# Kernel optimization log

Measured on AMD Instinct MI355X. Metric: run time of the kernel, lower is better.

Reference implementation:

```python
import jax, jax.numpy as jnp
import numpy as np

B, T, D, E, C = 2, 2048, 2048, 8, 512
O1 = D // E  # per-expert hidden width (out_features // num_experts)


def setup_inputs() -> dict:
    key = jax.random.key(0)
    k = jax.random.split(key, 8)
    s = 1.0 / np.sqrt(D)
    return {
        "x": jax.random.normal(k[0], (B, T, D), dtype=jnp.float32),
        "dispatch_mask": jax.random.uniform(k[1], (B, T, E, C), dtype=jnp.float32),
        "combine_array": jax.random.uniform(k[2], (B, T, E, C), dtype=jnp.float32),
        # contract weights: nn.Linear(D, D) reshaped to (E, D//E, D)
        "W1": jax.random.uniform(k[3], (E, O1, D), jnp.float32, -s, s),
        "b1": jax.random.uniform(k[4], (E, O1), jnp.float32, -s, s),
        # expand weights: nn.Linear(D, D) reshaped to (E, D, D//E)
        "W2": jax.random.uniform(k[5], (E, D, O1), jnp.float32, -s, s),
        "b2": jax.random.uniform(k[6], (D,), jnp.float32, -s, s),
    }


def reference(x, dispatch_mask, combine_array, W1, b1, W2, b2):
    # --- ExpertsChooseMaskedContract ---
    # einsum('btd,btec,eod->beco') split into two GEMM-shaped contractions
    xe = jnp.einsum('btd,btec->becd', x, dispatch_mask)          # [B,E,C,D]
    h = jnp.einsum('becd,eod->beco', xe, W1) + b1[None, :, None, :]  # [B,E,C,O1]
    # --- GELU (torch nn.GELU default = exact erf form) ---
    h = jax.nn.gelu(h, approximate=False)
    # --- ExpertsChooseMaskedExpand (homogeneous-coords bias == add b2 then combine) ---
    y = jnp.einsum('beci,eoi->beco', h, W2) + b2[None, None, None, :]  # [B,E,C,D]
    out = jnp.einsum('beco,btec->bto', y, combine_array)          # [B,T,D]
    return out
```

## Files before the change

### kernel.cpp

```cpp
#include <hip/hip_runtime.h>
#include <math.h>

#define BB 2
#define TT 2048
#define DD 2048
#define EE 8
#define CCv 512
#define OO1 256

typedef unsigned short u16;
typedef __bf16 bf16x8 __attribute__((ext_vector_type(8)));
typedef float f32x4 __attribute__((ext_vector_type(4)));

__device__ __forceinline__ u16 f2bf(float f) {
    unsigned u = __float_as_uint(f);
    unsigned r = (u + 0x7fffu + ((u >> 16) & 1u)) >> 16;
    return (u16)r;
}

__device__ __forceinline__ void gload16(const void* g, void* s) {
    __builtin_amdgcn_global_load_lds(
        (const __attribute__((address_space(1))) void*)g,
        (__attribute__((address_space(3))) void*)s, 16, 0, 0);
}

__global__ __launch_bounds__(256) void conv_cast(const float* __restrict__ in,
                                                 u16* __restrict__ out, long n) {
    long i = ((long)blockIdx.x * 256 + threadIdx.x) * 4;
    float4 v = *(const float4*)&in[i];
    ushort4 o; o.x = f2bf(v.x); o.y = f2bf(v.y); o.z = f2bf(v.z); o.w = f2bf(v.w);
    *(ushort4*)&out[i] = o;
}

__global__ __launch_bounds__(256) void transpose_conv(
    const float* __restrict__ in, long inHi, long inLo, int modZ, long sIn,
    u16* __restrict__ out, long outZ, long sOut)
{
    __shared__ float tile[32][33];
    const int z = blockIdx.z;
    const float* ib = in + (long)(z / modZ) * inHi + (long)(z % modZ) * inLo;
    u16* ob = out + (long)z * outZ;
    const int t0 = blockIdx.y * 32, c0 = blockIdx.x * 32;
    const int tid = threadIdx.x;
    const int r = tid >> 3, c4 = (tid & 7) * 4;

    float4 v = *(const float4*)&ib[(long)(t0 + r) * sIn + c0 + c4];
    tile[r][c4 + 0] = v.x; tile[r][c4 + 1] = v.y;
    tile[r][c4 + 2] = v.z; tile[r][c4 + 3] = v.w;
    __syncthreads();

    const int oc = tid >> 3, t4 = (tid & 7) * 4;
    ushort4 o;
    o.x = f2bf(tile[t4 + 0][oc]);
    o.y = f2bf(tile[t4 + 1][oc]);
    o.z = f2bf(tile[t4 + 2][oc]);
    o.w = f2bf(tile[t4 + 3][oc]);
    *(ushort4*)&ob[(long)(c0 + oc) * sOut + t0 + t4] = o;
}

template<int EPI>
__global__ __launch_bounds__(256)
void mfma_gemm(const u16* __restrict__ A, long ldA, long aHi, long aLo, int modA,
               const u16* __restrict__ B, long ldB, long bHi, long bLo, int modB,
               void* __restrict__ Cout, long ldC, long cHi, long cLo, int modC,
               const float* __restrict__ bias, long biasLo, int modBias,
               int M, int N, int K)
{
    __shared__ __align__(16) char smem[32768];
    char* smA = smem;
    char* smB = smem + 16384;

    const int z = blockIdx.z;
    const char* Ab = (const char*)(A + (long)(z / modA) * aHi + (long)(z % modA) * aLo);
    const char* Bb = (const char*)(B + (long)(z / modB) * bHi + (long)(z % modB) * bLo);
    const long ldAb = ldA * 2, ldBb = ldB * 2;

    const int m0 = blockIdx.y * 128, n0 = blockIdx.x * 128;
    const int tid = threadIdx.x;
    const int l = tid & 63;
    const int w = tid >> 6;
    const int wm = w >> 1, wn = w & 1;

    const int srow = l >> 3;
    const int schunk = (l & 7) ^ srow;
    const int frow = l & 15;
    const int fgrp = l >> 4;
    const int fch0 = fgrp ^ (l & 7);

    int aoff[4], boff[4];
#pragma unroll
    for (int i = 0; i < 4; ++i) {
        aoff[i] = (wm * 64 + i * 16 + frow) * 128 + fch0 * 16;
        boff[i] = (wn * 64 + i * 16 + frow) * 128 + fch0 * 16;
    }

    f32x4 acc[4][4];
    const f32x4 zero4 = {0.f, 0.f, 0.f, 0.f};
#pragma unroll
    for (int i = 0; i < 4; ++i)
#pragma unroll
        for (int j = 0; j < 4; ++j) acc[i][j] = zero4;

    const long sgo = (long)schunk * 16;

    for (int k0 = 0; k0 < K; k0 += 64) {
        const long kb = (long)k0 * 2;
#pragma unroll
        for (int j = 0; j < 4; ++j) {
            const int rr = (j * 4 + w) * 8 + srow;
            gload16(Ab + (long)(m0 + rr) * ldAb + kb + sgo, smA + (j * 4 + w) * 1024);
            gload16(Bb + (long)(n0 + rr) * ldBb + kb + sgo, smB + (j * 4 + w) * 1024);
        }
        __syncthreads();
#pragma unroll
        for (int kk = 0; kk < 2; ++kk) {
            const int kx = kk * 64;
            bf16x8 af[4], bfr[4];
#pragma unroll
            for (int i = 0; i < 4; ++i) af[i] = *(const bf16x8*)(smA + (aoff[i] ^ kx));
#pragma unroll
            for (int i = 0; i < 4; ++i) bfr[i] = *(const bf16x8*)(smB + (boff[i] ^ kx));
#pragma unroll
            for (int mi = 0; mi < 4; ++mi)
#pragma unroll
                for (int ni = 0; ni < 4; ++ni)
                    acc[mi][ni] = __builtin_amdgcn_mfma_f32_16x16x32_bf16(
                        af[mi], bfr[ni], acc[mi][ni], 0, 0, 0);
        }
        __syncthreads();
    }

    const long cbase = (long)(z / modC) * cHi + (long)(z % modC) * cLo;
    const float* biasB = bias + (long)(z % modBias) * biasLo;
#pragma unroll
    for (int mi = 0; mi < 4; ++mi) {
#pragma unroll
        for (int ni = 0; ni < 4; ++ni) {
            const int col = n0 + wn * 64 + ni * 16 + frow;
            const int rowb = m0 + wm * 64 + mi * 16 + fgrp * 4;
#pragma unroll
            for (int r = 0; r < 4; ++r) {
                float v = acc[mi][ni][r];
                const int row = rowb + r;
                if (EPI == 1) {
                    v += biasB[col];
                    v = 0.5f * v * (1.0f + erff(v * 0.70710678118654752f));
                } else {
                    v += biasB[row];
                }
                ((u16*)Cout)[cbase + (long)row * ldC + col] = f2bf(v);
            }
        }
    }
}

template<int OUTBF>
__global__ __launch_bounds__(512, 2)
void mfma_gemm_big(const u16* __restrict__ A, long ldA, long aHi, long aLo, int modA,
                   const u16* __restrict__ B, long ldB, long bHi, long bLo, int modB,
                   void* __restrict__ Cout, long ldC, long cHi, long cLo, int modC,
                   int M, int N, int K)
{
    __shared__ __align__(16) char smem[147456];

    const int z = blockIdx.z;
    const char* Ab = (const char*)(A + (long)(z / modA) * aHi + (long)(z % modA) * aLo);
    const char* Bb = (const char*)(B + (long)(z / modB) * bHi + (long)(z % modB) * bLo);
    const long ldAb = ldA * 2, ldBb = ldB * 2;

    const int m0 = blockIdx.y * 256, n0 = blockIdx.x * 128;
    const int tid = threadIdx.x;
    const int l = tid & 63;
    const int w = tid >> 6;
    const int wm = w >> 1, wn = w & 1;

    const int srow = l >> 3;
    const int schunk = (l & 7) ^ srow;
    const long sgo = (long)schunk * 16;
    const int frow = l & 15;
    const int fgrp = l >> 4;
    const int fsw = (fgrp ^ (l & 7)) * 16;

    auto stageA = [&](int kt, int bsel, int j) {
        const int rr = (j * 8 + w) * 8 + srow;
        gload16(Ab + (long)(m0 + rr) * ldAb + (long)kt * 128 + sgo,
                smem + bsel * 49152 + (j * 8 + w) * 1024);
    };
    auto stageB = [&](int kt, int bsel, int j) {
        const int rr = (j * 8 + w) * 8 + srow;
        gload16(Bb + (long)(n0 + rr) * ldBb + (long)kt * 128 + sgo,
                smem + bsel * 49152 + 32768 + (j * 8 + w) * 1024);
    };

    f32x4 acc[4][4];
    const f32x4 zero4 = {0.f, 0.f, 0.f, 0.f};
#pragma unroll
    for (int i = 0; i < 4; ++i)
#pragma unroll
        for (int j = 0; j < 4; ++j) acc[i][j] = zero4;

#pragma unroll
    for (int j = 0; j < 4; ++j) stageA(0, 0, j);
#pragma unroll
    for (int j = 0; j < 2; ++j) stageB(0, 0, j);
#pragma unroll
    for (int j = 0; j < 4; ++j) stageA(1, 1, j);
#pragma unroll
    for (int j = 0; j < 2; ++j) stageB(1, 1, j);
    asm volatile("s_waitcnt vmcnt(6)" ::: "memory");
    __builtin_amdgcn_s_barrier();

    const int NT = K >> 6;
    int bc = 0;
    int sc = 2;
    for (int kt = 0; kt < NT; ++kt) {
        const char* bufA = smem + bc * 49152;
        const char* bufB = bufA + 32768;
        const bool pf = (kt + 2) < NT;

        if (pf) {
            const int kpf = kt + 2;
            stageA(kpf, sc, 0); stageA(kpf, sc, 1);
            stageA(kpf, sc, 2); stageA(kpf, sc, 3);
            stageB(kpf, sc, 0); stageB(kpf, sc, 1);
        }

        bf16x8 af[4][2], bfr[4][2];
#pragma unroll
        for (int mi = 0; mi < 4; ++mi) {
            const int ab = (wm * 64 + mi * 16 + frow) * 128 + fsw;
            af[mi][0] = *(const bf16x8*)(bufA + ab);
            af[mi][1] = *(const bf16x8*)(bufA + (ab ^ 64));
        }
#pragma unroll
        for (int ni = 0; ni < 4; ++ni) {
            const int bb = (wn * 64 + ni * 16 + frow) * 128 + fsw;
            bfr[ni][0] = *(const bf16x8*)(bufB + bb);
            bfr[ni][1] = *(const bf16x8*)(bufB + (bb ^ 64));
        }

        __builtin_amdgcn_s_setprio(1);
#pragma unroll
        for (int kk = 0; kk < 2; ++kk)
#pragma unroll
            for (int mi = 0; mi < 4; ++mi)
#pragma unroll
                for (int ni = 0; ni < 4; ++ni)
                    acc[mi][ni] = __builtin_amdgcn_mfma_f32_16x16x32_bf16(
                        af[mi][kk], bfr[ni][kk], acc[mi][ni], 0, 0, 0);
        __builtin_amdgcn_s_setprio(0);

        if (pf) { asm volatile("s_waitcnt vmcnt(6)" ::: "memory"); }
        else    { asm volatile("s_waitcnt vmcnt(0)" ::: "memory"); }
        __builtin_amdgcn_s_barrier();

        bc = (bc == 2) ? 0 : bc + 1;
        sc = (sc == 2) ? 0 : sc + 1;
    }

    const long cbase = (long)(z / modC) * cHi + (long)(z % modC) * cLo;
#pragma unroll
    for (int mi = 0; mi < 4; ++mi) {
#pragma unroll
        for (int ni = 0; ni < 4; ++ni) {
            const int col = n0 + wn * 64 + ni * 16 + frow;
            const int rowb = m0 + wm * 64 + mi * 16 + fgrp * 4;
#pragma unroll
            for (int r = 0; r < 4; ++r) {
                const float v = acc[mi][ni][r];
                const long idx = cbase + (long)(rowb + r) * ldC + col;
                if (OUTBF) ((u16*)Cout)[idx] = f2bf(v);
                else       ((float*)Cout)[idx] = v;
            }
        }
    }
}

extern "C" void kernel_launch(void* const* d_in, const int* in_sizes, int n_in,
                              void* d_out, int out_size, void* d_ws, size_t ws_size,
                              hipStream_t stream) {
    const float* x    = (const float*)d_in[0];
    const float* mask = (const float*)d_in[1];
    const float* comb = (const float*)d_in[2];
    const float* W1   = (const float*)d_in[3];
    const float* b1   = (const float*)d_in[4];
    const float* W2   = (const float*)d_in[5];
    const float* b2   = (const float*)d_in[6];
    float* out = (float*)d_out;

    char* ws = (char*)d_ws;
    u16* buf0 = (u16*)ws;
    u16* xT   = (u16*)(ws + 33554432);
    u16* W1b  = (u16*)(ws + 50331648);
    u16* W2b  = (u16*)(ws + 58720256);
    u16* xe   = (u16*)(ws + 67108864);
    u16* h    = (u16*)(ws + 100663296);
    u16* yT   = xe;

    transpose_conv<<<dim3(DD / 32, TT / 32, BB), 256, 0, stream>>>(
        x, (long)TT * DD, 0L, 1, (long)DD, xT, (long)DD * TT, (long)TT);
    transpose_conv<<<dim3(CCv / 32, TT / 32, BB * EE), 256, 0, stream>>>(
        mask, (long)TT * EE * CCv, (long)CCv, EE, (long)EE * CCv,
        buf0, (long)CCv * TT, (long)TT);
    conv_cast<<<(int)((8L * OO1 * DD) / 1024), 256, 0, stream>>>(W1, W1b, 8L * OO1 * DD);
    conv_cast<<<(int)((8L * DD * OO1) / 1024), 256, 0, stream>>>(W2, W2b, 8L * DD * OO1);

    mfma_gemm_big<1><<<dim3(DD / 128, CCv / 256, 16), 512, 0, stream>>>(
        buf0, 2048, 1048576L, 0L, 1,
        xT,   2048, 4194304L, 0L, 8,
        xe,   2048, 1048576L, 0L, 1,
        CCv, DD, TT);

    conv_cast<<<(int)((2L * TT * EE * CCv) / 1024), 256, 0, stream>>>(
        comb, buf0, 2L * TT * EE * CCv);

    mfma_gemm<1><<<dim3(OO1 / 128, CCv / 128, 16), 256, 0, stream>>>(
        xe,  2048, 1048576L, 0L, 1,
        W1b, 2048, 0L, 524288L, 8,
        h,   256, 131072L, 0L, 1,
        b1, 256L, 8, CCv, OO1, DD);

    mfma_gemm<3><<<dim3(CCv / 128, DD / 128, 16), 256, 0, stream>>>(
        W2b, 256, 0L, 524288L, 8,
        h,   256, 131072L, 0L, 1,
        yT,  4096, 8388608L, 512L, 8,
        b2, 0L, 1, DD, CCv, OO1);

    mfma_gemm_big<0><<<dim3(DD / 128, TT / 256, BB), 512, 0, stream>>>(
        buf0, 4096, 8388608L, 0L, 1,
        yT,   4096, 8388608L, 0L, 1,
        out,  2048, 4194304L, 0L, 1,
        TT, DD, EE * CCv);
}
```

Baseline: 277.2 us.

## Split GEMM k-loop into two half-phases interleaving LDS reads, prefetch, and MFMA

Splits each k-tile iteration of the bf16 MFMA GEMM into two halves. Each half loads its LDS fragments, issues part of the global-to-LDS prefetch, synchronises with a barrier, and runs 16 MFMAs. LDS fragment offsets are hoisted out of the loop. The aim is to overlap LDS reads and global prefetch issue with matrix-core work, in exchange for an extra block barrier per iteration, explicit lgkmcnt waits, and sched_barrier constraints on the compiler.

```diff
diff --git a/kernel.cpp b/kernel.cpp
--- a/kernel.cpp
+++ b/kernel.cpp
@@ -199,6 +199,13 @@
 #pragma unroll
         for (int j = 0; j < 4; ++j) acc[i][j] = zero4;
 
+    int aoff[4], boff[4];
+#pragma unroll
+    for (int i = 0; i < 4; ++i) {
+        aoff[i] = (wm * 64 + i * 16 + frow) * 128 + fsw;
+        boff[i] = (wn * 64 + i * 16 + frow) * 128 + fsw;
+    }
+
 #pragma unroll
     for (int j = 0; j < 4; ++j) stageA(0, 0, j);
 #pragma unroll
@@ -217,37 +224,42 @@
         const char* bufA = smem + bc * 49152;
         const char* bufB = bufA + 32768;
         const bool pf = (kt + 2) < NT;
-
-        if (pf) {
-            const int kpf = kt + 2;
-            stageA(kpf, sc, 0); stageA(kpf, sc, 1);
-            stageA(kpf, sc, 2); stageA(kpf, sc, 3);
-            stageB(kpf, sc, 0); stageB(kpf, sc, 1);
-        }
-
-        bf16x8 af[4][2], bfr[4][2];
-#pragma unroll
-        for (int mi = 0; mi < 4; ++mi) {
-            const int ab = (wm * 64 + mi * 16 + frow) * 128 + fsw;
-            af[mi][0] = *(const bf16x8*)(bufA + ab);
-            af[mi][1] = *(const bf16x8*)(bufA + (ab ^ 64));
-        }
-#pragma unroll
-        for (int ni = 0; ni < 4; ++ni) {
-            const int bb = (wn * 64 + ni * 16 + frow) * 128 + fsw;
-            bfr[ni][0] = *(const bf16x8*)(bufB + bb);
-            bfr[ni][1] = *(const bf16x8*)(bufB + (bb ^ 64));
-        }
-
+        const int kpf = kt + 2;
+
+        bf16x8 af0[4], bf0[4];
+#pragma unroll
+        for (int mi = 0; mi < 4; ++mi) af0[mi] = *(const bf16x8*)(bufA + aoff[mi]);
+#pragma unroll
+        for (int ni = 0; ni < 4; ++ni) bf0[ni] = *(const bf16x8*)(bufB + boff[ni]);
+        if (pf) { stageA(kpf, sc, 0); stageA(kpf, sc, 1); stageA(kpf, sc, 2); }
+        __builtin_amdgcn_s_barrier();
+        asm volatile("s_waitcnt lgkmcnt(0)" ::: "memory");
+        __builtin_amdgcn_sched_barrier(0);
         __builtin_amdgcn_s_setprio(1);
 #pragma unroll
-        for (int kk = 0; kk < 2; ++kk)
-#pragma unroll
-            for (int mi = 0; mi < 4; ++mi)
-#pragma unroll
-                for (int ni = 0; ni < 4; ++ni)
-                    acc[mi][ni] = __builtin_amdgcn_mfma_f32_16x16x32_bf16(
-                        af[mi][kk], bfr[ni][kk], acc[mi][ni], 0, 0, 0);
+        for (int mi = 0; mi < 4; ++mi)
+#pragma unroll
+            for (int ni = 0; ni < 4; ++ni)
+                acc[mi][ni] = __builtin_amdgcn_mfma_f32_16x16x32_bf16(
+                    af0[mi], bf0[ni], acc[mi][ni], 0, 0, 0);
+        __builtin_amdgcn_s_setprio(0);
+
+        bf16x8 af1[4], bf1[4];
+#pragma unroll
+        for (int mi = 0; mi < 4; ++mi) af1[mi] = *(const bf16x8*)(bufA + (aoff[mi] ^ 64));
+#pragma unroll
+        for (int ni = 0; ni < 4; ++ni) bf1[ni] = *(const bf16x8*)(bufB + (boff[ni] ^ 64));
+        if (pf) { stageA(kpf, sc, 3); stageB(kpf, sc, 0); stageB(kpf, sc, 1); }
+        __builtin_amdgcn_s_barrier();
+        asm volatile("s_waitcnt lgkmcnt(0)" ::: "memory");
+        __builtin_amdgcn_sched_barrier(0);
+        __builtin_amdgcn_s_setprio(1);
+#pragma unroll
+        for (int mi = 0; mi < 4; ++mi)
+#pragma unroll
+            for (int ni = 0; ni < 4; ++ni)
+                acc[mi][ni] = __builtin_amdgcn_mfma_f32_16x16x32_bf16(
+                    af1[mi], bf1[ni], acc[mi][ni], 0, 0, 0);
         __builtin_amdgcn_s_setprio(0);
 
         if (pf) { asm volatile("s_waitcnt vmcnt(6)" ::: "memory"); }
```

After: 280.6 us. No clear change (+1.2%).
